# Optimization experiments

Hardware: AMD Instinct MI355X
Metric: run time of the kernel (lower is better)

The kernel has to match this reference:

```python
import jax, jax.numpy as jnp
import numpy as np

N_NODES = 50000
N_RAND_EDGES = 800000
LEAKY_SLOPE = 0.2


def gat_layer(x, edge_index, W, a_src, a_dst, b, num_heads):
    """Multi-head GAT layer. W: [Din, Dout]; heads split Dout; concat output."""
    N = x.shape[0]
    Dout = W.shape[1]
    Dh = Dout // num_heads
    z = (x @ W).reshape(N, num_heads, Dh)                      # [N,H,Dh]
    src = edge_index[0]
    dst = edge_index[1]
    alpha_src = jnp.einsum('nhd,hd->nh', z, a_src)             # [N,H]
    alpha_dst = jnp.einsum('nhd,hd->nh', z, a_dst)             # [N,H]
    e = jax.nn.leaky_relu(alpha_src[src] + alpha_dst[dst], LEAKY_SLOPE)  # [E,H]
    # segment softmax over incoming edges of each dst node
    m = jax.ops.segment_max(e, dst, num_segments=N)            # [N,H]
    e = jnp.exp(e - m[dst])
    denom = jax.ops.segment_sum(e, dst, num_segments=N)        # [N,H]
    alpha = e / (denom[dst] + 1e-16)                           # [E,H]
    msg = z[src] * alpha[:, :, None]                           # [E,H,Dh]
    out = jax.ops.segment_sum(msg, dst, num_segments=N)        # [N,H,Dh]
    return out.reshape(N, Dout) + b


def setup_inputs() -> dict:
    key = jax.random.key(0)
    ks = jax.random.split(key, 12)
    input_dim, hidden_dim, num_classes, num_heads = 128, 64, 16, 8
    x = jax.random.normal(ks[0], (N_NODES, input_dim), dtype=jnp.float32)
    rand_edges = jax.random.randint(ks[1], (2, N_RAND_EDGES), 0, N_NODES, dtype=jnp.int32)
    self_loops = jnp.tile(jnp.arange(N_NODES, dtype=jnp.int32), (2, 1))
    edge_indices = jnp.concatenate([rand_edges, self_loops], axis=1)   # [2, 850000]

    def glorot(k, shape):
        fan = sum(shape[-2:]) if len(shape) > 1 else shape[0]
        return jax.random.normal(k, shape, dtype=jnp.float32) * (2.0 / fan) ** 0.5

    W1 = glorot(ks[2], (input_dim, hidden_dim))
    a_src1 = glorot(ks[3], (num_heads, hidden_dim // num_heads))
    a_dst1 = glorot(ks[4], (num_heads, hidden_dim // num_heads))
    b1 = jnp.zeros((hidden_dim,), dtype=jnp.float32)
    W2 = glorot(ks[5], (hidden_dim, num_classes))
    a_src2 = glorot(ks[6], (1, num_classes))
    a_dst2 = glorot(ks[7], (1, num_classes))
    b2 = jnp.zeros((num_classes,), dtype=jnp.float32)
    return {"x": x, "edge_indices": edge_indices,
            "W1": W1, "a_src1": a_src1, "a_dst1": a_dst1, "b1": b1,
            "W2": W2, "a_src2": a_src2, "a_dst2": a_dst2, "b2": b2}


def reference(x, edge_indices, W1, a_src1, a_dst1, b1, W2, a_src2, a_dst2, b2):
    # Dropout is identity in eval mode.
    h = gat_layer(x, edge_indices, W1, a_src1, a_dst1, b1, num_heads=8)
    h = jax.nn.elu(h)
    return gat_layer(h, edge_indices, W2, a_src2, a_dst2, b2, num_heads=1)
```

## Files before the change

kernel.cpp:

```cpp
#include <hip/hip_runtime.h>
#include <hip/hip_fp16.h>


#define LRELU(v) ((v) > 0.f ? (v) : 0.2f * (v))

#define NB   196
#define BCAP 5120

typedef _Float16 f16x8 __attribute__((ext_vector_type(8)));
typedef float f32x4 __attribute__((ext_vector_type(4)));

__global__ void __launch_bounds__(256, 4)
kA(const float* __restrict__ x, const float* __restrict__ W1,
   const float* __restrict__ a_dst1,
   const int* __restrict__ src, const int* __restrict__ dst,
   int* __restrict__ bcnt, int* __restrict__ pairs,
   __half* __restrict__ z1h, float* __restrict__ ad1, int N, int E) {
    __shared__ __half xsh[64][136];
    __shared__ __half wtT[64][136];
    __shared__ float avs[64];
    int b = blockIdx.x;
    int tid = threadIdx.x;
    bool is_part = ((b % 5) == 4);

    if (is_part) {
        int* hist  = (int*)&xsh[0][0];
        int* base_ = hist + 256;
        int* cur   = hist + 512;
        int rank = b / 5;
        if (tid < NB) hist[tid] = 0;
        __syncthreads();
        int chunk = (E + NB - 1) / NB;
        int e0 = rank * chunk;
        int e1 = min(e0 + chunk, E);
        for (int e = e0 + tid; e < e1; e += 256)
            atomicAdd(&hist[dst[e] >> 8], 1);
        __syncthreads();
        if (tid < NB) {
            base_[tid] = atomicAdd(&bcnt[tid], hist[tid]);
            cur[tid] = 0;
        }
        __syncthreads();
        for (int e = e0 + tid; e < e1; e += 256) {
            int d = dst[e], s = src[e];
            int bk = d >> 8;
            int r = atomicAdd(&cur[bk], 1);
            int idx = base_[bk] + r;
            if (idx < BCAP) pairs[bk * BCAP + idx] = (s << 8) | (d & 255);
        }
        return;
    }

    int tile = (b / 5) * 4 + (b % 5);
    if (tile >= 782) return;
    int n0 = tile * 64;
    for (int idx = tid; idx < 2048; idx += 256) {
        int r = idx >> 5, q = idx & 31;
        int n = n0 + r; if (n >= N) n = N - 1;
        float4 v = ((const float4*)(x + (size_t)n * 128))[q];
        union { __half2 h2[2]; uint2 u; } pk;
        pk.h2[0] = __floats2half2_rn(v.x, v.y);
        pk.h2[1] = __floats2half2_rn(v.z, v.w);
        *(uint2*)&xsh[r][q * 4] = pk.u;
    }
    for (int idx = tid; idx < 1024; idx += 256) {
        int kp = idx >> 4, cq = idx & 15;
        float4 va = ((const float4*)(W1 + (size_t)(kp * 2) * 64))[cq];
        float4 vb = ((const float4*)(W1 + (size_t)(kp * 2 + 1) * 64))[cq];
        int c = cq * 4;
        *(__half2*)&wtT[c + 0][kp * 2] = __floats2half2_rn(va.x, vb.x);
        *(__half2*)&wtT[c + 1][kp * 2] = __floats2half2_rn(va.y, vb.y);
        *(__half2*)&wtT[c + 2][kp * 2] = __floats2half2_rn(va.z, vb.z);
        *(__half2*)&wtT[c + 3][kp * 2] = __floats2half2_rn(va.w, vb.w);
    }
    if (tid < 64) avs[tid] = a_dst1[tid];
    __syncthreads();

    int lane = tid & 63, wv = tid >> 6;
    int rsub = lane & 15, kg = lane >> 4;
    f32x4 acc0 = {0.f, 0.f, 0.f, 0.f}, acc1 = {0.f, 0.f, 0.f, 0.f};
    f32x4 acc2 = {0.f, 0.f, 0.f, 0.f}, acc3 = {0.f, 0.f, 0.f, 0.f};
#pragma unroll
    for (int k0 = 0; k0 < 128; k0 += 32) {
        f16x8 av = *(const f16x8*)&xsh[wv * 16 + rsub][k0 + kg * 8];
        f16x8 b0 = *(const f16x8*)&wtT[rsub][k0 + kg * 8];
        f16x8 b1 = *(const f16x8*)&wtT[16 + rsub][k0 + kg * 8];
        f16x8 b2 = *(const f16x8*)&wtT[32 + rsub][k0 + kg * 8];
        f16x8 b3 = *(const f16x8*)&wtT[48 + rsub][k0 + kg * 8];
        acc0 = __builtin_amdgcn_mfma_f32_16x16x32_f16(av, b0, acc0, 0, 0, 0);
        acc1 = __builtin_amdgcn_mfma_f32_16x16x32_f16(av, b1, acc1, 0, 0, 0);
        acc2 = __builtin_amdgcn_mfma_f32_16x16x32_f16(av, b2, acc2, 0, 0, 0);
        acc3 = __builtin_amdgcn_mfma_f32_16x16x32_f16(av, b3, acc3, 0, 0, 0);
    }
#pragma unroll
    for (int reg = 0; reg < 4; ++reg) {
        int n = n0 + wv * 16 + kg * 4 + reg;
        if (n < N) {
            __half* zp = z1h + (size_t)n * 64 + rsub;
            zp[0]  = __float2half_rn(acc0[reg]);
            zp[16] = __float2half_rn(acc1[reg]);
            zp[32] = __float2half_rn(acc2[reg]);
            zp[48] = __float2half_rn(acc3[reg]);
        }
        float v0 = acc0[reg] * avs[rsub];
        float v1 = acc1[reg] * avs[16 + rsub];
        float v2 = acc2[reg] * avs[32 + rsub];
        float v3 = acc3[reg] * avs[48 + rsub];
        v0 += __shfl_xor(v0, 1, 64); v0 += __shfl_xor(v0, 2, 64); v0 += __shfl_xor(v0, 4, 64);
        v1 += __shfl_xor(v1, 1, 64); v1 += __shfl_xor(v1, 2, 64); v1 += __shfl_xor(v1, 4, 64);
        v2 += __shfl_xor(v2, 1, 64); v2 += __shfl_xor(v2, 2, 64); v2 += __shfl_xor(v2, 4, 64);
        v3 += __shfl_xor(v3, 1, 64); v3 += __shfl_xor(v3, 2, 64); v3 += __shfl_xor(v3, 4, 64);
        if ((rsub & 7) == 0 && n < N) {
            int hi = rsub >> 3;
            float* ap = ad1 + (size_t)n * 8 + hi;
            ap[0] = v0; ap[2] = v1; ap[4] = v2; ap[6] = v3;
        }
    }
}

__global__ void kB(const int* __restrict__ bcnt, const int* __restrict__ pairs,
                   int* __restrict__ deg, int* __restrict__ csr, int N) {
    __shared__ int cur[256];
    int b = blockIdx.x;
    int tid = threadIdx.x;
    cur[tid] = 0;
    __syncthreads();
    int nb = min(bcnt[b], BCAP);
    const int* p = pairs + b * BCAP;
    for (int i = tid; i < nb; i += 256) {
        int v = p[i];
        int off = v & 255, s = v >> 8;
        int r = atomicAdd(&cur[off], 1);
        if (r < 64) csr[(((b << 8) + off) << 6) + r] = s;
    }
    __syncthreads();
    int d = (b << 8) + tid;
    if (d < N) deg[d] = cur[tid];
}

__global__ void kg1(const int* __restrict__ deg, const int* __restrict__ csr,
                    const float* __restrict__ a_src1, const float* __restrict__ ad1,
                    const __half* __restrict__ z1h, const float* __restrict__ b1,
                    const float* __restrict__ W2, const float* __restrict__ a_src2,
                    const float* __restrict__ a_dst2,
                    float* __restrict__ z2r, int N) {
    __shared__ int s_idx[16][65];
    __shared__ int sdeg[16];
    __shared__ float hs[4][4][68];
    __shared__ float ws2[64][18];
    int tid = threadIdx.x;
    int lane = tid & 63, wid = tid >> 6;
    int blk0 = blockIdx.x * 16;
    for (int i = tid; i < 1024; i += 256) ws2[i >> 4][i & 15] = W2[i];
    for (int idx = tid; idx < 1024; idx += 256) {
        int dl = idx >> 6, sl = idx & 63;
        int dr = blk0 + dl; if (dr >= N) dr = N - 1;
        s_idx[dl][sl] = csr[(dr << 6) + sl];
    }
    if (tid < 16) {
        int dr = blk0 + tid; if (dr >= N) dr = N - 1;
        sdeg[tid] = min(deg[dr], 64);
    }
    __syncthreads();

    int dloc = lane >> 4, g = (lane >> 3) & 1, q = lane & 7;
    int dl16 = wid * 4 + dloc;
    int d = blk0 + dl16;
    int dc = d < N ? d : N - 1;
    int cnt = d < N ? sdeg[dl16] : 0;
    float adv = ad1[(size_t)dc * 8 + q];
    float4 asA = *(const float4*)(a_src1 + q * 8);
    float4 asB = *(const float4*)(a_src1 + q * 8 + 4);
    float a0 = 0.f, a1 = 0.f, a2 = 0.f, a3 = 0.f;
    float a4 = 0.f, a5 = 0.f, a6 = 0.f, a7 = 0.f, dsum = 0.f;
#pragma unroll 2
    for (int j = g; j < cnt; j += 2) {
        int s = s_idx[dl16][j];
        float4 raw = *(const float4*)(z1h + (size_t)s * 64 + q * 8);
        const __half2* hp = (const __half2*)&raw;
        float2 f0 = __half22float2(hp[0]), f1 = __half22float2(hp[1]);
        float2 f2 = __half22float2(hp[2]), f3 = __half22float2(hp[3]);
        float av = f0.x * asA.x + f0.y * asA.y + f1.x * asA.z + f1.y * asA.w
                 + f2.x * asB.x + f2.y * asB.y + f3.x * asB.z + f3.y * asB.w;
        float ev = av + adv;
        float w = __expf(LRELU(ev));
        a0 += w * f0.x; a1 += w * f0.y; a2 += w * f1.x; a3 += w * f1.y;
        a4 += w * f2.x; a5 += w * f2.y; a6 += w * f3.x; a7 += w * f3.y;
        dsum += w;
    }
    a0 += __shfl_xor(a0, 8, 64); a1 += __shfl_xor(a1, 8, 64);
    a2 += __shfl_xor(a2, 8, 64); a3 += __shfl_xor(a3, 8, 64);
    a4 += __shfl_xor(a4, 8, 64); a5 += __shfl_xor(a5, 8, 64);
    a6 += __shfl_xor(a6, 8, 64); a7 += __shfl_xor(a7, 8, 64);
    dsum += __shfl_xor(dsum, 8, 64);
    float inv = cnt ? 1.f / dsum : 0.f;
    float4 bv0 = *(const float4*)(b1 + q * 8);
    float4 bv1 = *(const float4*)(b1 + q * 8 + 4);
    float hv[8] = {a0 * inv + bv0.x, a1 * inv + bv0.y,
                   a2 * inv + bv0.z, a3 * inv + bv0.w,
                   a4 * inv + bv1.x, a5 * inv + bv1.y,
                   a6 * inv + bv1.z, a7 * inv + bv1.w};
#pragma unroll
    for (int i = 0; i < 8; ++i) hv[i] = hv[i] > 0.f ? hv[i] : expm1f(hv[i]);
    if (g == 0) {
        *(float4*)&hs[wid][dloc][q * 8]     = make_float4(hv[0], hv[1], hv[2], hv[3]);
        *(float4*)&hs[wid][dloc][q * 8 + 4] = make_float4(hv[4], hv[5], hv[6], hv[7]);
    }
    float zc0 = 0.f, zc1 = 0.f;
#pragma unroll
    for (int k4 = 0; k4 < 16; ++k4) {
        float4 hh = *(const float4*)&hs[wid][dloc][k4 * 4];
        float2 w0 = *(const float2*)&ws2[k4 * 4 + 0][q * 2];
        float2 w1 = *(const float2*)&ws2[k4 * 4 + 1][q * 2];
        float2 w2 = *(const float2*)&ws2[k4 * 4 + 2][q * 2];
        float2 w3 = *(const float2*)&ws2[k4 * 4 + 3][q * 2];
        zc0 += hh.x * w0.x; zc1 += hh.x * w0.y;
        zc0 += hh.y * w1.x; zc1 += hh.y * w1.y;
        zc0 += hh.z * w2.x; zc1 += hh.z * w2.y;
        zc0 += hh.w * w3.x; zc1 += hh.w * w3.y;
    }
    if (g == 0 && d < N)
        *(float2*)&z2r[(size_t)d * 32 + q * 2] = make_float2(zc0, zc1);
    float ps = zc0 * a_src2[q * 2] + zc1 * a_src2[q * 2 + 1];
    float pd = zc0 * a_dst2[q * 2] + zc1 * a_dst2[q * 2 + 1];
#pragma unroll
    for (int m = 1; m < 8; m <<= 1) {
        ps += __shfl_xor(ps, m, 64);
        pd += __shfl_xor(pd, m, 64);
    }
    if (q == 0 && g == 0 && d < N) {
        z2r[(size_t)d * 32 + 16] = ps;
        z2r[(size_t)d * 32 + 17] = pd;
    }
}

__global__ void kg2(const int* __restrict__ deg, const int* __restrict__ csr,
                    const float* __restrict__ z2r, const float* __restrict__ b2,
                    float* __restrict__ out, int N) {
    __shared__ int s_idx[16][65];
    __shared__ int sdeg[16];
    int tid = threadIdx.x;
    int lane = tid & 63, wid = tid >> 6;
    int blk0 = blockIdx.x * 16;
    for (int idx = tid; idx < 1024; idx += 256) {
        int dl = idx >> 6, sl = idx & 63;
        int dr = blk0 + dl; if (dr >= N) dr = N - 1;
        s_idx[dl][sl] = csr[(dr << 6) + sl];
    }
    if (tid < 16) {
        int dr = blk0 + tid; if (dr >= N) dr = N - 1;
        sdeg[tid] = min(deg[dr], 64);
    }
    __syncthreads();

    int dloc = lane >> 4, g = (lane >> 2) & 3, c = lane & 3;
    int dl16 = wid * 4 + dloc;
    int d = blk0 + dl16;
    int dc = d < N ? d : N - 1;
    int cnt = d < N ? sdeg[dl16] : 0;
    float adv = z2r[(size_t)dc * 32 + 17];
    float ax = 0.f, ay = 0.f, az = 0.f, aw = 0.f, dsum = 0.f;
#pragma unroll 2
    for (int j = g; j < cnt; j += 4) {
        int s = s_idx[dl16][j];
        float as2v = z2r[(size_t)s * 32 + 16];
        float ev = as2v + adv;
        float w = __expf(LRELU(ev));
        float4 zv = *(const float4*)(z2r + (size_t)s * 32 + c * 4);
        ax += w * zv.x; ay += w * zv.y; az += w * zv.z; aw += w * zv.w;
        dsum += w;
    }
#pragma unroll
    for (int m = 4; m <= 8; m <<= 1) {
        ax += __shfl_xor(ax, m, 64); ay += __shfl_xor(ay, m, 64);
        az += __shfl_xor(az, m, 64); aw += __shfl_xor(aw, m, 64);
        dsum += __shfl_xor(dsum, m, 64);
    }
    if (g == 0 && d < N) {
        float inv = 1.f / dsum;
        float4 o = make_float4(ax * inv + b2[c * 4], ay * inv + b2[c * 4 + 1],
                               az * inv + b2[c * 4 + 2], aw * inv + b2[c * 4 + 3]);
        *(float4*)&out[(size_t)d * 16 + c * 4] = o;
    }
}

extern "C" void kernel_launch(void* const* d_in, const int* in_sizes, int n_in,
                              void* d_out, int out_size, void* d_ws, size_t ws_size,
                              hipStream_t stream) {
    const float* x      = (const float*)d_in[0];
    const int*   ei     = (const int*)d_in[1];
    const float* W1     = (const float*)d_in[2];
    const float* a_src1 = (const float*)d_in[3];
    const float* a_dst1 = (const float*)d_in[4];
    const float* b1     = (const float*)d_in[5];
    const float* W2     = (const float*)d_in[6];
    const float* a_src2 = (const float*)d_in[7];
    const float* a_dst2 = (const float*)d_in[8];
    const float* b2     = (const float*)d_in[9];
    float* out = (float*)d_out;

    const int N = in_sizes[0] / 128;
    const int E = in_sizes[1] / 2;
    const int* src = ei;
    const int* dst = ei + E;

    float* ws = (float*)d_ws;
    size_t off = 0;
    __half* z1h = (__half*)(ws + off); off += (size_t)N * 32;
    float* ad1 = ws + off; off += (size_t)N * 8;
    float* z2r = ws + off; off += (size_t)N * 32;
    int* csr = (int*)(ws + off); off += (size_t)N * 64;
    int* deg = (int*)(ws + off); off += (size_t)N;
    int* pairs = (int*)(ws + off); off += (size_t)NB * BCAP;
    int* bcnt = (int*)(ws + off); off += NB;

    hipMemsetAsync(bcnt, 0, (size_t)NB * sizeof(int), stream);

    kA<<<980, 256, 0, stream>>>(x, W1, a_dst1, src, dst, bcnt, pairs,
                                z1h, ad1, N, E);
    kB<<<NB, 256, 0, stream>>>(bcnt, pairs, deg, csr, N);
    kg1<<<(N + 15) / 16, 256, 0, stream>>>(deg, csr, a_src1, ad1, z1h, b1, W2,
                                           a_src2, a_dst2, z2r, N);
    kg2<<<(N + 15) / 16, 256, 0, stream>>>(deg, csr, z2r, b2, out, N);
}
```

Measured before the change: 158.3 us.

## Use per-rank private bucket slots instead of global atomic offsets; widen kg1 edge split

The partition blocks now write edges into private (bucket, rank) slots of fixed capacity, with no histogram pass and no global atomicAdd on shared bucket counters. The memset of the counters also goes away. kB rebuilds the order with a shared-memory prefix scan over per-rank counts and a binary search per element. kg1 handles 8 destinations per block with 4 edge-groups per destination instead of 2, which raises parallelism per node at the cost of an extra shuffle-reduction step and twice as many blocks. The cost is a much larger pairs buffer, extra search work in kB, and possible overflow if any rank-bucket pair exceeds 512 entries.

After: 169.2 us. +6.9%, slower.

```diff
diff --git a/kernel.cpp b/kernel.cpp
--- a/kernel.cpp
+++ b/kernel.cpp
@@ -5,7 +5,7 @@
 #define LRELU(v) ((v) > 0.f ? (v) : 0.2f * (v))
 
 #define NB   196
-#define BCAP 5120
+#define CAP  512
 
 typedef _Float16 f16x8 __attribute__((ext_vector_type(8)));
 typedef float f32x4 __attribute__((ext_vector_type(4)));
@@ -14,7 +14,7 @@
 kA(const float* __restrict__ x, const float* __restrict__ W1,
    const float* __restrict__ a_dst1,
    const int* __restrict__ src, const int* __restrict__ dst,
-   int* __restrict__ bcnt, int* __restrict__ pairs,
+   int* __restrict__ cnts, int* __restrict__ pairs,
    __half* __restrict__ z1h, float* __restrict__ ad1, int N, int E) {
     __shared__ __half xsh[64][136];
     __shared__ __half wtT[64][136];
@@ -24,30 +24,21 @@
     bool is_part = ((b % 5) == 4);
 
     if (is_part) {
-        int* hist  = (int*)&xsh[0][0];
-        int* base_ = hist + 256;
-        int* cur   = hist + 512;
+        int* cur = (int*)&xsh[0][0];
         int rank = b / 5;
-        if (tid < NB) hist[tid] = 0;
+        if (tid < NB) cur[tid] = 0;
         __syncthreads();
         int chunk = (E + NB - 1) / NB;
         int e0 = rank * chunk;
         int e1 = min(e0 + chunk, E);
-        for (int e = e0 + tid; e < e1; e += 256)
-            atomicAdd(&hist[dst[e] >> 8], 1);
-        __syncthreads();
-        if (tid < NB) {
-            base_[tid] = atomicAdd(&bcnt[tid], hist[tid]);
-            cur[tid] = 0;
-        }
-        __syncthreads();
         for (int e = e0 + tid; e < e1; e += 256) {
             int d = dst[e], s = src[e];
             int bk = d >> 8;
-            int r = atomicAdd(&cur[bk], 1);
-            int idx = base_[bk] + r;
-            if (idx < BCAP) pairs[bk * BCAP + idx] = (s << 8) | (d & 255);
+            int i = atomicAdd(&cur[bk], 1);
+            if (i < CAP) pairs[((bk * NB + rank) << 9) + i] = (s << 8) | (d & 255);
         }
+        __syncthreads();
+        if (tid < NB) cnts[tid * NB + rank] = min(cur[tid], CAP);
         return;
     }
 
@@ -118,20 +109,35 @@
     }
 }
 
-__global__ void kB(const int* __restrict__ bcnt, const int* __restrict__ pairs,
+__global__ void kB(const int* __restrict__ cnts, const int* __restrict__ pairs,
                    int* __restrict__ deg, int* __restrict__ csr, int N) {
     __shared__ int cur[256];
+    __shared__ int pref[256];
     int b = blockIdx.x;
     int tid = threadIdx.x;
     cur[tid] = 0;
-    __syncthreads();
-    int nb = min(bcnt[b], BCAP);
-    const int* p = pairs + b * BCAP;
+    pref[tid] = (tid < NB) ? cnts[b * NB + tid] : 0;
+    __syncthreads();
+    for (int offs = 1; offs < 256; offs <<= 1) {
+        int add = (tid >= offs) ? pref[tid - offs] : 0;
+        __syncthreads();
+        pref[tid] += add;
+        __syncthreads();
+    }
+    int nb = pref[255];
+    const int* p = pairs + ((size_t)b * NB << 9);
     for (int i = tid; i < nb; i += 256) {
-        int v = p[i];
+        int lo = 0, hi = 255;
+        while (lo < hi) {
+            int mid = (lo + hi) >> 1;
+            if (pref[mid] > i) hi = mid; else lo = mid + 1;
+        }
+        int r = lo;
+        int base = r ? pref[r - 1] : 0;
+        int v = p[(r << 9) + (i - base)];
         int off = v & 255, s = v >> 8;
-        int r = atomicAdd(&cur[off], 1);
-        if (r < 64) csr[(((b << 8) + off) << 6) + r] = s;
+        int pos = atomicAdd(&cur[off], 1);
+        if (pos < 64) csr[(((b << 8) + off) << 6) + pos] = s;
     }
     __syncthreads();
     int d = (b << 8) + tid;
@@ -144,38 +150,38 @@
                     const float* __restrict__ W2, const float* __restrict__ a_src2,
                     const float* __restrict__ a_dst2,
                     float* __restrict__ z2r, int N) {
-    __shared__ int s_idx[16][65];
-    __shared__ int sdeg[16];
-    __shared__ float hs[4][4][68];
+    __shared__ int s_idx[8][65];
+    __shared__ int sdeg[8];
+    __shared__ float hs[4][2][68];
     __shared__ float ws2[64][18];
     int tid = threadIdx.x;
     int lane = tid & 63, wid = tid >> 6;
-    int blk0 = blockIdx.x * 16;
+    int blk0 = blockIdx.x * 8;
     for (int i = tid; i < 1024; i += 256) ws2[i >> 4][i & 15] = W2[i];
-    for (int idx = tid; idx < 1024; idx += 256) {
+    for (int idx = tid; idx < 512; idx += 256) {
         int dl = idx >> 6, sl = idx & 63;
         int dr = blk0 + dl; if (dr >= N) dr = N - 1;
         s_idx[dl][sl] = csr[(dr << 6) + sl];
     }
-    if (tid < 16) {
+    if (tid < 8) {
         int dr = blk0 + tid; if (dr >= N) dr = N - 1;
         sdeg[tid] = min(deg[dr], 64);
     }
     __syncthreads();
 
-    int dloc = lane >> 4, g = (lane >> 3) & 1, q = lane & 7;
-    int dl16 = wid * 4 + dloc;
-    int d = blk0 + dl16;
+    int dloc = lane >> 5, g = (lane >> 3) & 3, q = lane & 7;
+    int dl8 = wid * 2 + dloc;
+    int d = blk0 + dl8;
     int dc = d < N ? d : N - 1;
-    int cnt = d < N ? sdeg[dl16] : 0;
+    int cnt = d < N ? sdeg[dl8] : 0;
     float adv = ad1[(size_t)dc * 8 + q];
     float4 asA = *(const float4*)(a_src1 + q * 8);
     float4 asB = *(const float4*)(a_src1 + q * 8 + 4);
     float a0 = 0.f, a1 = 0.f, a2 = 0.f, a3 = 0.f;
     float a4 = 0.f, a5 = 0.f, a6 = 0.f, a7 = 0.f, dsum = 0.f;
 #pragma unroll 2
-    for (int j = g; j < cnt; j += 2) {
-        int s = s_idx[dl16][j];
+    for (int j = g; j < cnt; j += 4) {
+        int s = s_idx[dl8][j];
         float4 raw = *(const float4*)(z1h + (size_t)s * 64 + q * 8);
         const __half2* hp = (const __half2*)&raw;
         float2 f0 = __half22float2(hp[0]), f1 = __half22float2(hp[1]);
@@ -188,11 +194,14 @@
         a4 += w * f2.x; a5 += w * f2.y; a6 += w * f3.x; a7 += w * f3.y;
         dsum += w;
     }
-    a0 += __shfl_xor(a0, 8, 64); a1 += __shfl_xor(a1, 8, 64);
-    a2 += __shfl_xor(a2, 8, 64); a3 += __shfl_xor(a3, 8, 64);
-    a4 += __shfl_xor(a4, 8, 64); a5 += __shfl_xor(a5, 8, 64);
-    a6 += __shfl_xor(a6, 8, 64); a7 += __shfl_xor(a7, 8, 64);
-    dsum += __shfl_xor(dsum, 8, 64);
+#pragma unroll
+    for (int m = 8; m <= 16; m <<= 1) {
+        a0 += __shfl_xor(a0, m, 64); a1 += __shfl_xor(a1, m, 64);
+        a2 += __shfl_xor(a2, m, 64); a3 += __shfl_xor(a3, m, 64);
+        a4 += __shfl_xor(a4, m, 64); a5 += __shfl_xor(a5, m, 64);
+        a6 += __shfl_xor(a6, m, 64); a7 += __shfl_xor(a7, m, 64);
+        dsum += __shfl_xor(dsum, m, 64);
+    }
     float inv = cnt ? 1.f / dsum : 0.f;
     float4 bv0 = *(const float4*)(b1 + q * 8);
     float4 bv1 = *(const float4*)(b1 + q * 8 + 4);
@@ -311,15 +320,13 @@
     float* z2r = ws + off; off += (size_t)N * 32;
     int* csr = (int*)(ws + off); off += (size_t)N * 64;
     int* deg = (int*)(ws + off); off += (size_t)N;
-    int* pairs = (int*)(ws + off); off += (size_t)NB * BCAP;
-    int* bcnt = (int*)(ws + off); off += NB;
-
-    hipMemsetAsync(bcnt, 0, (size_t)NB * sizeof(int), stream);
-
-    kA<<<980, 256, 0, stream>>>(x, W1, a_dst1, src, dst, bcnt, pairs,
+    int* pairs = (int*)(ws + off); off += (size_t)NB * NB * CAP;
+    int* cnts = (int*)(ws + off); off += (size_t)NB * NB;
+
+    kA<<<980, 256, 0, stream>>>(x, W1, a_dst1, src, dst, cnts, pairs,
                                 z1h, ad1, N, E);
-    kB<<<NB, 256, 0, stream>>>(bcnt, pairs, deg, csr, N);
-    kg1<<<(N + 15) / 16, 256, 0, stream>>>(deg, csr, a_src1, ad1, z1h, b1, W2,
-                                           a_src2, a_dst2, z2r, N);
+    kB<<<NB, 256, 0, stream>>>(cnts, pairs, deg, csr, N);
+    kg1<<<(N + 7) / 8, 256, 0, stream>>>(deg, csr, a_src1, ad1, z1h, b1, W2,
+                                         a_src2, a_dst2, z2r, N);
     kg2<<<(N + 15) / 16, 256, 0, stream>>>(deg, csr, z2r, b2, out, N);
 }
```
